# Kernel tuning notes

Hardware: AMD Instinct MI355X
Metric: run time of the kernel (lower is better)

## Reference

```python
import jax, jax.numpy as jnp
import numpy as np

B, P, C, F = 16, 1000, 91, 1024      # images, proposals/img, classes (incl bg), box-head dim
H, W = 800, 800                      # image shape (all images same size)
SCORE_THRESH = 0.05
NMS_THRESH = 0.5
DETS = 100                           # detections_per_img
MIN_SIZE = 1e-2
BBOX_XFORM_CLIP = float(np.log(1000.0 / 16.0))
OFF = float(max(H, W) + 2)           # class offset unit for batched (class-aware) NMS


def setup_inputs() -> dict:
    key = jax.random.key(0)
    k1, k2, k3, k4 = jax.random.split(key, 4)
    box_features = jax.random.normal(k1, (B * P, F), jnp.float32)
    Wc = jax.random.normal(k2, (F, C), jnp.float32) * 0.02
    bc = jnp.zeros((C,), jnp.float32)
    Wb = jax.random.normal(k3, (F, C * 4), jnp.float32) * 0.02
    bb = jnp.zeros((C * 4,), jnp.float32)
    u = jax.random.uniform(k4, (B, P, 4), jnp.float32)
    x1 = u[..., 0] * (W * 0.8)
    y1 = u[..., 1] * (H * 0.8)
    x2 = x1 + 16.0 + u[..., 2] * (W * 0.2)
    y2 = y1 + 16.0 + u[..., 3] * (H * 0.2)
    proposals = jnp.stack([x1, y1, x2, y2], axis=-1)
    return dict(box_features=box_features, Wc=Wc, bc=bc, Wb=Wb, bb=bb,
                proposals=proposals)


def _decode_and_clip(regs, props):
    # regs: [N, C, 4] deltas; props: [N, 4] xyxy. bbox_reg_weights = (1,1,1,1).
    w = props[:, 2] - props[:, 0]
    h = props[:, 3] - props[:, 1]
    cx = props[:, 0] + 0.5 * w
    cy = props[:, 1] + 0.5 * h
    dx, dy = regs[..., 0], regs[..., 1]
    dw = jnp.minimum(regs[..., 2], BBOX_XFORM_CLIP)
    dh = jnp.minimum(regs[..., 3], BBOX_XFORM_CLIP)
    pcx = dx * w[:, None] + cx[:, None]
    pcy = dy * h[:, None] + cy[:, None]
    pw = jnp.exp(dw) * w[:, None]
    ph = jnp.exp(dh) * h[:, None]
    x1 = jnp.clip(pcx - 0.5 * pw, 0.0, float(W))
    y1 = jnp.clip(pcy - 0.5 * ph, 0.0, float(H))
    x2 = jnp.clip(pcx + 0.5 * pw, 0.0, float(W))
    y2 = jnp.clip(pcy + 0.5 * ph, 0.0, float(H))
    return jnp.stack([x1, y1, x2, y2], axis=-1)  # [N, C, 4]


def _iou_one_vs_all(box, boxes):
    ix1 = jnp.maximum(box[0], boxes[:, 0])
    iy1 = jnp.maximum(box[1], boxes[:, 1])
    ix2 = jnp.minimum(box[2], boxes[:, 2])
    iy2 = jnp.minimum(box[3], boxes[:, 3])
    inter = jnp.clip(ix2 - ix1, 0.0) * jnp.clip(iy2 - iy1, 0.0)
    a1 = (box[2] - box[0]) * (box[3] - box[1])
    a2 = (boxes[:, 2] - boxes[:, 0]) * (boxes[:, 3] - boxes[:, 1])
    return inter / (a1 + a2 - inter + 1e-9)


def _greedy_nms(boxes, scores):
    # boxes: [M,4] (class-offset), scores: [M] (-inf = filtered out).
    # Returns selected indices [DETS] and scores [DETS] (0 where no valid pick).
    def body(i, st):
        sc, sel, ss = st
        j = jnp.argmax(sc)
        s = sc[j]
        iou = _iou_one_vs_all(boxes[j], boxes)
        sc = jnp.where(iou > NMS_THRESH, -jnp.inf, sc)  # suppresses j itself too
        valid = s > 0.0
        sel = sel.at[i].set(jnp.where(valid, j.astype(jnp.int32), 0))
        ss = ss.at[i].set(jnp.where(valid, s, 0.0))
        return sc, sel, ss
    init = (scores, jnp.zeros((DETS,), jnp.int32), jnp.zeros((DETS,), jnp.float32))
    _, sel, ss = jax.lax.fori_loop(0, DETS, body, init)
    return sel, ss


def reference(box_features, Wc, bc, Wb, bb, proposals):
    # Box predictor (FastRCNNPredictor-style linear heads).
    class_logits = box_features @ Wc + bc                  # [B*P, C]
    box_regression = (box_features @ Wb + bb).reshape(-1, C, 4)
    # Decode per-class boxes against proposals, clip to image.
    pred = _decode_and_clip(box_regression, proposals.reshape(-1, 4))  # [B*P, C, 4]
    scores = jax.nn.softmax(class_logits, axis=-1)         # [B*P, C]
    # Drop background class 0; flatten (proposal, class) per image.
    M = P * (C - 1)
    boxes_all = pred[:, 1:, :].reshape(B, M, 4)
    scores_all = scores[:, 1:].reshape(B, M)
    labels_all = jnp.tile(jnp.arange(1, C, dtype=jnp.int32), P)  # [M]
    # Score threshold + remove tiny boxes (mask instead of dynamic filter).
    bw = boxes_all[..., 2] - boxes_all[..., 0]
    bh = boxes_all[..., 3] - boxes_all[..., 1]
    keep = (scores_all > SCORE_THRESH) & (bw >= MIN_SIZE) & (bh >= MIN_SIZE)
    scores_m = jnp.where(keep, scores_all, -jnp.inf)
    # Class-aware batched NMS via per-class coordinate offsets.
    boxes_off = boxes_all + (labels_all.astype(jnp.float32) * OFF)[None, :, None]
    sel, det_scores = jax.vmap(_greedy_nms)(boxes_off, scores_m)   # [B,DETS]
    det_boxes = jnp.take_along_axis(boxes_all, sel[..., None], axis=1)  # [B,DETS,4]
    det_labels = labels_all[sel]                                        # [B,DETS]
    valid = det_scores > 0.0
    det_boxes = det_boxes * valid[..., None]
    det_labels = jnp.where(valid, det_labels, 0)
    return det_boxes, det_scores, det_labels
```

## Files before the change

### kernel.cpp

```cpp
#include <hip/hip_runtime.h>
#include <hip/hip_bf16.h>
#include <math.h>

typedef unsigned long long ull;

#define BB_ 16
#define PP_ 1000
#define CC_ 91
#define FF_ 1024
#define DETS_ 100
#define CAP_ 2048
#define CAND_MAX (BB_ * CAP_)
#define SURV_CAP 2048
#define CLS_CAP 256
#define BLK_CAND 720
#define IMG_W 800.0f
#define IMG_H 800.0f
#define OFF_ 802.0f
#define SCORE_TH 0.05f
#define PRE_TH 0.047f
#define NMS_TH 0.5f
#define MIN_SZ 0.01f
#define BBOX_CLIP_D 4.135166556742356

__global__ __launch_bounds__(256) void wb_transpose(
    const float* __restrict__ Wb, float* __restrict__ Wbt)
{
    const int idx = blockIdx.x * 256 + threadIdx.x;
    if (idx >= CC_ * 4 * FF_) return;
    const int c = idx >> 12;
    const int j = (idx >> 10) & 3;
    const int k = idx & 1023;
    if (c < 1) { Wbt[idx] = 0.f; return; }
    Wbt[idx] = Wb[(size_t)k * (CC_ * 4) + 4 * c + j];
}

__global__ __launch_bounds__(512) void prepass_rows(
    const float* __restrict__ A, const float* __restrict__ Wc,
    const float* __restrict__ bc,
    int* __restrict__ rowlist, int* __restrict__ nrowsp)
{
    __shared__ union __align__(16) SM {
        struct { float Af[2][16][34]; float Bs[2][16][98]; } t;
        float Ssc[32][97];
    } sm;
    __shared__ float comb[256][12];

    const int tid = threadIdx.x;
    const int kg = tid >> 8;
    const int l = tid & 255;
    const int row0 = blockIdx.x * 32;
    const int kbase = kg * 512;
    const int ty2 = (l >> 4) * 2;
    const int tx6 = (l & 15) * 6;

    const int am = l >> 2;
    const int ak = (l & 3) * 4;
    const int bk = l >> 4;
    const int bn = (l & 15) * 6;

    float acc[2][6];
#pragma unroll
    for (int i = 0; i < 2; ++i)
#pragma unroll
        for (int j = 0; j < 6; ++j) acc[i][j] = 0.f;

    float4 avP = make_float4(0.f, 0.f, 0.f, 0.f);
    if (l < 128)
        avP = *reinterpret_cast<const float4*>(
            A + (size_t)(row0 + am) * FF_ + kbase + ak);
    float bvP[6];
#pragma unroll
    for (int jj = 0; jj < 6; ++jj) {
        const int c = bn + jj;
        bvP[jj] = (c < CC_) ? Wc[(size_t)(kbase + bk) * CC_ + c] : 0.f;
    }

    for (int k0 = 0; k0 < 512; k0 += 16) {
        if (l < 128) {
            sm.t.Af[kg][ak + 0][am] = avP.x;
            sm.t.Af[kg][ak + 1][am] = avP.y;
            sm.t.Af[kg][ak + 2][am] = avP.z;
            sm.t.Af[kg][ak + 3][am] = avP.w;
        }
#pragma unroll
        for (int jj = 0; jj < 6; ++jj) sm.t.Bs[kg][bk][bn + jj] = bvP[jj];

        const int kn = k0 + 16;
        if (kn < 512) {
            if (l < 128)
                avP = *reinterpret_cast<const float4*>(
                    A + (size_t)(row0 + am) * FF_ + kbase + kn + ak);
#pragma unroll
            for (int jj = 0; jj < 6; ++jj) {
                const int c = bn + jj;
                bvP[jj] = (c < CC_) ? Wc[(size_t)(kbase + kn + bk) * CC_ + c] : 0.f;
            }
        }
        __syncthreads();

#pragma unroll
        for (int k = 0; k < 16; ++k) {
            const float2 af = *reinterpret_cast<const float2*>(&sm.t.Af[kg][k][ty2]);
            const float2 b01 = *reinterpret_cast<const float2*>(&sm.t.Bs[kg][k][tx6 + 0]);
            const float2 b23 = *reinterpret_cast<const float2*>(&sm.t.Bs[kg][k][tx6 + 2]);
            const float2 b45 = *reinterpret_cast<const float2*>(&sm.t.Bs[kg][k][tx6 + 4]);
            const float a0 = af.x, a1 = af.y;
            acc[0][0] += a0 * b01.x; acc[0][1] += a0 * b01.y;
            acc[0][2] += a0 * b23.x; acc[0][3] += a0 * b23.y;
            acc[0][4] += a0 * b45.x; acc[0][5] += a0 * b45.y;
            acc[1][0] += a1 * b01.x; acc[1][1] += a1 * b01.y;
            acc[1][2] += a1 * b23.x; acc[1][3] += a1 * b23.y;
            acc[1][4] += a1 * b45.x; acc[1][5] += a1 * b45.y;
        }
        __syncthreads();
    }

    if (kg == 1) {
#pragma unroll
        for (int i = 0; i < 2; ++i)
#pragma unroll
            for (int j = 0; j < 6; ++j) comb[l][i * 6 + j] = acc[i][j];
    }
    __syncthreads();
    if (kg == 0) {
#pragma unroll
        for (int i = 0; i < 2; ++i)
#pragma unroll
            for (int j = 0; j < 6; ++j) {
                const int c = tx6 + j;
                if (c < CC_)
                    sm.Ssc[ty2 + i][c] = acc[i][j] + comb[l][i * 6 + j] + bc[c];
            }
    }
    __syncthreads();

    if (tid < 32) {
        float m_all = sm.Ssc[tid][0];
        float m_fg = -INFINITY;
        for (int c = 1; c < CC_; ++c) {
            const float lv = sm.Ssc[tid][c];
            m_all = fmaxf(m_all, lv);
            m_fg = fmaxf(m_fg, lv);
        }
        float denom = 0.f;
        for (int c = 0; c < CC_; ++c) denom += expf(sm.Ssc[tid][c] - m_all);
        const float maxsc = expf(m_fg - m_all) / denom;
        if (maxsc > PRE_TH) {
            const int pos = atomicAdd(nrowsp, 1);
            rowlist[pos] = row0 + tid;
        }
    }
}

template<bool USE_T>
__global__ __launch_bounds__(512) void logits_fp64_rows(
    const float* __restrict__ A, const float* __restrict__ Wc,
    const float* __restrict__ bc,
    const float* __restrict__ Wb, const float* __restrict__ Wbt,
    const float* __restrict__ bb, const float* __restrict__ props,
    const int* __restrict__ rowlist, const int* __restrict__ nrowsp,
    float* __restrict__ cs, int* __restrict__ clab,
    int* __restrict__ corig, int* __restrict__ cpidx,
    int* __restrict__ cnt,
    float* __restrict__ cx1, float* __restrict__ cy1,
    float* __restrict__ cx2, float* __restrict__ cy2)
{
    const int nr = *nrowsp;
    const int row0 = blockIdx.x * 8;
    if (row0 >= nr) return;

    __shared__ union __align__(16) SM {
        struct { float Af[2][16][12]; float Bs[2][16][98]; } t;
        struct { int cp[BLK_CAND]; int cc[BLK_CAND]; int cg[BLK_CAND]; } d;
    } sm;
    __shared__ __align__(16) double dcomb[256][3];
    __shared__ float Ssc[8][97];
    __shared__ int ncand;

    const int tid = threadIdx.x;
    const int kg = tid >> 8;
    const int l = tid & 255;
    const int kbase = kg * 512;
    const int r = l >> 5;
    const int c0 = (l & 31) * 3;

    if (tid == 0) ncand = 0;

    const int aslot = l >> 2;
    const int akq = (l & 3) * 4;
    const float* Arow = nullptr;
    if (l < 32) {
        const int ridx = min(row0 + aslot, nr - 1);
        Arow = A + (size_t)rowlist[ridx] * FF_ + kbase;
    }
    const int bk = l >> 4;
    const int bn = (l & 15) * 6;

    double acc[3] = {0.0, 0.0, 0.0};

    float4 avP = make_float4(0.f, 0.f, 0.f, 0.f);
    if (l < 32) avP = *reinterpret_cast<const float4*>(Arow + akq);
    float bvP[6];
#pragma unroll
    for (int jj = 0; jj < 6; ++jj) {
        const int c = bn + jj;
        bvP[jj] = (c < CC_) ? Wc[(size_t)(kbase + bk) * CC_ + c] : 0.f;
    }

    for (int k0 = 0; k0 < 512; k0 += 16) {
        if (l < 32) {
            sm.t.Af[kg][akq + 0][aslot] = avP.x;
            sm.t.Af[kg][akq + 1][aslot] = avP.y;
            sm.t.Af[kg][akq + 2][aslot] = avP.z;
            sm.t.Af[kg][akq + 3][aslot] = avP.w;
        }
#pragma unroll
        for (int jj = 0; jj < 6; ++jj) sm.t.Bs[kg][bk][bn + jj] = bvP[jj];

        const int kn = k0 + 16;
        if (kn < 512) {
            if (l < 32)
                avP = *reinterpret_cast<const float4*>(Arow + kn + akq);
#pragma unroll
            for (int jj = 0; jj < 6; ++jj) {
                const int c = bn + jj;
                bvP[jj] = (c < CC_) ? Wc[(size_t)(kbase + kn + bk) * CC_ + c] : 0.f;
            }
        }
        __syncthreads();

#pragma unroll
        for (int k = 0; k < 16; ++k) {
            const double a0 = (double)sm.t.Af[kg][k][r];
            const double b0 = (double)sm.t.Bs[kg][k][c0 + 0];
            const double b1 = (double)sm.t.Bs[kg][k][c0 + 1];
            const double b2 = (double)sm.t.Bs[kg][k][c0 + 2];
            acc[0] += a0 * b0;
            acc[1] += a0 * b1;
            acc[2] += a0 * b2;
        }
        __syncthreads();
    }

    if (kg == 1) {
#pragma unroll
        for (int j = 0; j < 3; ++j) dcomb[l][j] = acc[j];
    }
    __syncthreads();
    if (kg == 0) {
#pragma unroll
        for (int j = 0; j < 3; ++j) {
            const int c = c0 + j;
            if (c < CC_) {
                const double v = acc[j] + dcomb[l][j];
                Ssc[r][c] = __fadd_rn((float)v, bc[c]);
            }
        }
    }
    __syncthreads();

    {
        const int w = tid >> 6;
        const int lane = tid & 63;
        if (w < 8 && row0 + w < nr) {
            const int p = rowlist[row0 + w];
            const int b = p / PP_;
            const int pi = p - b * PP_;

            const float l1 = Ssc[w][lane];
            const float l2 = (lane < CC_ - 64) ? Ssc[w][lane + 64] : -INFINITY;
            float m = fmaxf(l1, l2);
#pragma unroll
            for (int off = 32; off > 0; off >>= 1)
                m = fmaxf(m, __shfl_xor(m, off));

            double d = exp((double)l1 - (double)m);
            if (lane < CC_ - 64) d += exp((double)l2 - (double)m);
#pragma unroll
            for (int off = 1; off < 64; off <<= 1)
                d += __shfl_xor(d, off);

#pragma unroll
            for (int q = 0; q < 2; ++q) {
                const int c = lane + q * 64;
                if (c >= 1 && c < CC_) {
                    const double sd = exp((double)Ssc[w][c] - (double)m) / d;
                    const float score = (float)sd;
                    if (score > SCORE_TH) {
                        const int pos = atomicAdd(&cnt[b], 1);
                        if (pos < CAP_) {
                            const int g = b * CAP_ + pos;
                            cs[g] = score;
                            clab[g] = c;
                            corig[g] = pi * (CC_ - 1) + (c - 1);
                            cpidx[g] = p;
                            const int slot = atomicAdd(&ncand, 1);
                            if (slot < BLK_CAND) {
                                sm.d.cp[slot] = p;
                                sm.d.cc[slot] = c;
                                sm.d.cg[slot] = g;
                            }
                        }
                    }
                }
            }
        }
    }
    __syncthreads();

    {
        const int w = tid >> 6;
        const int lane = tid & 63;
        const int nc = min(ncand, BLK_CAND);
        for (int ci = w; ci < nc; ci += 8) {
            const int p = sm.d.cp[ci];
            const int c = sm.d.cc[ci];
            const int g = sm.d.cg[ci];

            const float* fr = A + (size_t)p * FF_;
            double a0 = 0.0, a1 = 0.0, a2 = 0.0, a3 = 0.0;
            if (USE_T) {
                const float* w0 = Wbt + (size_t)c * 4096;
                for (int k = lane; k < FF_; k += 64) {
                    const double f = (double)fr[k];
                    a0 += f * (double)w0[k];
                    a1 += f * (double)w0[1024 + k];
                    a2 += f * (double)w0[2048 + k];
                    a3 += f * (double)w0[3072 + k];
                }
            } else {
                const float* wb0 = Wb + 4 * c;
                for (int k = lane; k < FF_; k += 64) {
                    const double f = (double)fr[k];
                    const float4 wv = *reinterpret_cast<const float4*>(
                        wb0 + (size_t)k * (CC_ * 4));
                    a0 += f * (double)wv.x; a1 += f * (double)wv.y;
                    a2 += f * (double)wv.z; a3 += f * (double)wv.w;
                }
            }
#pragma unroll
            for (int off = 32; off > 0; off >>= 1) {
                a0 += __shfl_xor(a0, off);
                a1 += __shfl_xor(a1, off);
                a2 += __shfl_xor(a2, off);
                a3 += __shfl_xor(a3, off);
            }

            if (lane == 0) {
                const float dx = __fadd_rn((float)a0, bb[4 * c + 0]);
                const float dy = __fadd_rn((float)a1, bb[4 * c + 1]);
                const float clipf = (float)BBOX_CLIP_D;
                const float dw = fminf(__fadd_rn((float)a2, bb[4 * c + 2]), clipf);
                const float dh = fminf(__fadd_rn((float)a3, bb[4 * c + 3]), clipf);

                const float px1 = props[(size_t)p * 4 + 0];
                const float py1 = props[(size_t)p * 4 + 1];
                const float px2 = props[(size_t)p * 4 + 2];
                const float py2 = props[(size_t)p * 4 + 3];
                const float wq = __fsub_rn(px2, px1);
                const float hq = __fsub_rn(py2, py1);
                const float cxq = __fadd_rn(px1, __fmul_rn(0.5f, wq));
                const float cyq = __fadd_rn(py1, __fmul_rn(0.5f, hq));

                const float pcx = __fadd_rn(__fmul_rn(dx, wq), cxq);
                const float pcy = __fadd_rn(__fmul_rn(dy, hq), cyq);
                const float ew = (float)exp((double)dw);
                const float eh = (float)exp((double)dh);
                const float pw = __fmul_rn(ew, wq);
                const float ph = __fmul_rn(eh, hq);

                const float hw = __fmul_rn(0.5f, pw);
                const float hh = __fmul_rn(0.5f, ph);
                const float bx1 = fminf(fmaxf(__fsub_rn(pcx, hw), 0.f), IMG_W);
                const float by1 = fminf(fmaxf(__fsub_rn(pcy, hh), 0.f), IMG_H);
                const float bx2 = fminf(fmaxf(__fadd_rn(pcx, hw), 0.f), IMG_W);
                const float by2 = fminf(fmaxf(__fadd_rn(pcy, hh), 0.f), IMG_H);

                cx1[g] = bx1; cy1[g] = by1; cx2[g] = bx2; cy2[g] = by2;
                if (!(__fsub_rn(bx2, bx1) >= MIN_SZ && __fsub_rn(by2, by1) >= MIN_SZ)) {
                    cs[g] = -INFINITY;
                }
            }
        }
    }
}

__global__ __launch_bounds__(64) void nms_class(
    const float* __restrict__ c_x1, const float* __restrict__ c_y1,
    const float* __restrict__ c_x2, const float* __restrict__ c_y2,
    const float* __restrict__ c_s, const int* __restrict__ c_lab,
    const int* __restrict__ c_orig, const int* __restrict__ cnt,
    ull* __restrict__ skey, float* __restrict__ sx1v, float* __restrict__ sy1v,
    float* __restrict__ sx2v, float* __restrict__ sy2v,
    int* __restrict__ slabv, int* __restrict__ scnt)
{
    const int blk = blockIdx.x;
    const int b = blk / (CC_ - 1);
    const int c = 1 + (blk - b * (CC_ - 1));
    const int lane = threadIdx.x;

    __shared__ ull kk[CLS_CAP];
    __shared__ float x1s[CLS_CAP], y1s[CLS_CAP], x2s[CLS_CAP], y2s[CLS_CAP];

    const int n = min(cnt[b], CAP_);

    int mcnt = 0;
    for (int i0 = 0; i0 < n; i0 += 64) {
        const int i = i0 + lane;
        bool take = false;
        float s = 0.f; int so = 0; int g = 0;
        if (i < n) {
            g = b * CAP_ + i;
            if (c_lab[g] == c) {
                s = c_s[g];
                if (s > 0.f) { take = true; so = c_orig[g]; }
            }
        }
        const ull bal = __ballot(take);
        if (take) {
            const int pos = mcnt + __popcll(bal & ((1ull << lane) - 1ull));
            if (pos < CLS_CAP) {
                kk[pos] = ((ull)__float_as_uint(s) << 32) |
                          (unsigned int)(0x7FFFFFFF - so);
                x1s[pos] = c_x1[g]; y1s[pos] = c_y1[g];
                x2s[pos] = c_x2[g]; y2s[pos] = c_y2[g];
            }
        }
        mcnt += (int)__popcll(bal);
    }
    mcnt = min(mcnt, CLS_CAP);
    if (mcnt == 0) return;
    __syncthreads();

    while (true) {
        ull best = 0ull;
        for (int i = lane; i < mcnt; i += 64) best = (kk[i] > best) ? kk[i] : best;
#pragma unroll
        for (int off = 32; off > 0; off >>= 1) {
            const ull o = __shfl_xor(best, off);
            best = (o > best) ? o : best;
        }
        if (best == 0ull) break;

        int wsl = -1;
        for (int i = lane; i < mcnt; i += 64) if (kk[i] == best) wsl = i;
        const ull bal = __ballot(wsl >= 0);
        const int wlane = (int)__ffsll((long long)bal) - 1;
        wsl = __shfl(wsl, wlane);

        const float wx1 = x1s[wsl], wy1 = y1s[wsl];
        const float wx2 = x2s[wsl], wy2 = y2s[wsl];

        if (lane == 0) {
            const int sp = atomicAdd(&scnt[b], 1);
            if (sp < SURV_CAP) {
                const int sg = b * SURV_CAP + sp;
                skey[sg] = best;
                sx1v[sg] = wx1; sy1v[sg] = wy1;
                sx2v[sg] = wx2; sy2v[sg] = wy2;
                slabv[sg] = c;
            }
        }

        const float off = __fmul_rn((float)c, OFF_);
        const float ax1 = __fadd_rn(wx1, off), ay1 = __fadd_rn(wy1, off);
        const float ax2 = __fadd_rn(wx2, off), ay2 = __fadd_rn(wy2, off);
        const float a1 = __fmul_rn(__fsub_rn(ax2, ax1), __fsub_rn(ay2, ay1));
        for (int i = lane; i < mcnt; i += 64) {
            if (kk[i] == 0ull) continue;
            const float bx1 = __fadd_rn(x1s[i], off), by1 = __fadd_rn(y1s[i], off);
            const float bx2 = __fadd_rn(x2s[i], off), by2 = __fadd_rn(y2s[i], off);
            const float ix1 = fmaxf(ax1, bx1), iy1 = fmaxf(ay1, by1);
            const float ix2 = fminf(ax2, bx2), iy2 = fminf(ay2, by2);
            const float inter = __fmul_rn(fmaxf(__fsub_rn(ix2, ix1), 0.f),
                                          fmaxf(__fsub_rn(iy2, iy1), 0.f));
            const float a2 = __fmul_rn(__fsub_rn(bx2, bx1), __fsub_rn(by2, by1));
            const float den = __fadd_rn(__fsub_rn(__fadd_rn(a1, a2), inter), 1e-9f);
            const float iou = __fdiv_rn(inter, den);
            if (iou > NMS_TH) kk[i] = 0ull;
        }
        __syncthreads();
    }
}

__global__ __launch_bounds__(256) void nms_merge(
    const ull* __restrict__ skey, const float* __restrict__ sx1v,
    const float* __restrict__ sy1v, const float* __restrict__ sx2v,
    const float* __restrict__ sy2v, const int* __restrict__ slabv,
    const int* __restrict__ scnt, float* __restrict__ out)
{
    const int b = blockIdx.x;
    const int t = threadIdx.x;

    __shared__ ull k_[SURV_CAP];
    __shared__ int id_[SURV_CAP];

    const int m = min(scnt[b], SURV_CAP);
    int N2 = 128;
    while (N2 < m) N2 <<= 1;

    for (int i = t; i < N2; i += 256) {
        k_[i] = (i < m) ? skey[b * SURV_CAP + i] : 0ull;
        id_[i] = i;
    }
    __syncthreads();

    for (int ksz = 2; ksz <= N2; ksz <<= 1) {
        for (int j = ksz >> 1; j > 0; j >>= 1) {
            for (int i = t; i < N2; i += 256) {
                const int ixj = i ^ j;
                if (ixj > i) {
                    const ull a = k_[i], cc = k_[ixj];
                    const bool desc = ((i & ksz) == 0);
                    if (desc ? (a < cc) : (a > cc)) {
                        k_[i] = cc; k_[ixj] = a;
                        const int tmp = id_[i]; id_[i] = id_[ixj]; id_[ixj] = tmp;
                    }
                }
            }
            __syncthreads();
        }
    }

    const int boxes_base = 0;
    const int scores_base = BB_ * DETS_ * 4;
    const int labels_base = BB_ * DETS_ * 5;

    for (int r = t; r < DETS_; r += 256) {
        const ull key = (r < N2) ? k_[r] : 0ull;
        float* bo = out + boxes_base + (size_t)(b * DETS_ + r) * 4;
        if (key != 0ull) {
            const int sg = b * SURV_CAP + id_[r];
            bo[0] = sx1v[sg]; bo[1] = sy1v[sg];
            bo[2] = sx2v[sg]; bo[3] = sy2v[sg];
            out[scores_base + b * DETS_ + r] = __uint_as_float((unsigned)(key >> 32));
            out[labels_base + b * DETS_ + r] = (float)slabv[sg];
        } else {
            bo[0] = 0.f; bo[1] = 0.f; bo[2] = 0.f; bo[3] = 0.f;
            out[scores_base + b * DETS_ + r] = 0.f;
            out[labels_base + b * DETS_ + r] = 0.f;
        }
    }
}

extern "C" void kernel_launch(void* const* d_in, const int* in_sizes, int n_in,
                              void* d_out, int out_size, void* d_ws, size_t ws_size,
                              hipStream_t stream)
{
    const float* feat  = (const float*)d_in[0];
    const float* Wc    = (const float*)d_in[1];
    const float* bc    = (const float*)d_in[2];
    const float* Wb    = (const float*)d_in[3];
    const float* bb    = (const float*)d_in[4];
    const float* props = (const float*)d_in[5];
    for (int i = 0; i < n_in; ++i) {
        const float* q = (const float*)d_in[i];
        switch (in_sizes[i]) {
            case 16384000: feat  = q; break;
            case 93184:    Wc    = q; break;
            case 91:       bc    = q; break;
            case 372736:   Wb    = q; break;
            case 364:      bb    = q; break;
            case 64000:    props = q; break;
        }
    }
    float* out = (float*)d_out;

    char* ws = (char*)d_ws;
    int*   cnt    = (int*)ws;
    int*   scnt   = (int*)(ws + 64);
    int*   nrowsp = (int*)(ws + 128);
    float* cs    = (float*)(ws + 256);
    int*   clab  = (int*)(cs + CAND_MAX);
    int*   corig = clab + CAND_MAX;
    int*   cpidx = corig + CAND_MAX;
    float* cx1   = (float*)(cpidx + CAND_MAX);
    float* cy1   = cx1 + CAND_MAX;
    float* cx2   = cy1 + CAND_MAX;
    float* cy2   = cx2 + CAND_MAX;
    ull*   skey  = (ull*)(cy2 + CAND_MAX);
    float* sx1v  = (float*)(skey + (size_t)BB_ * SURV_CAP);
    float* sy1v  = sx1v + (size_t)BB_ * SURV_CAP;
    float* sx2v  = sy1v + (size_t)BB_ * SURV_CAP;
    float* sy2v  = sx2v + (size_t)BB_ * SURV_CAP;
    int*   slabv = (int*)(sy2v + (size_t)BB_ * SURV_CAP);
    int*   rowlist = slabv + (size_t)BB_ * SURV_CAP;
    float* Wbt   = (float*)(rowlist + 16384);

    const size_t need = ((char*)(Wbt + CC_ * 4 * FF_)) - ws;
    const bool useT = (ws_size >= need);

    hipMemsetAsync(ws, 0, 256, stream);

    if (useT)
        wb_transpose<<<(CC_ * 4 * FF_ + 255) / 256, 256, 0, stream>>>(Wb, Wbt);

    prepass_rows<<<BB_ * PP_ / 32, 512, 0, stream>>>(feat, Wc, bc,
        rowlist, nrowsp);

    if (useT)
        logits_fp64_rows<true><<<BB_ * PP_ / 8, 512, 0, stream>>>(
            feat, Wc, bc, Wb, Wbt, bb, props, rowlist, nrowsp,
            cs, clab, corig, cpidx, cnt, cx1, cy1, cx2, cy2);
    else
        logits_fp64_rows<false><<<BB_ * PP_ / 8, 512, 0, stream>>>(
            feat, Wc, bc, Wb, Wbt, bb, props, rowlist, nrowsp,
            cs, clab, corig, cpidx, cnt, cx1, cy1, cx2, cy2);

    nms_class<<<BB_ * (CC_ - 1), 64, 0, stream>>>(
        cx1, cy1, cx2, cy2, cs, clab, corig, cnt,
        skey, sx1v, sy1v, sx2v, sy2v, slabv, scnt);

    nms_merge<<<BB_, 256, 0, stream>>>(
        skey, sx1v, sy1v, sx2v, sy2v, slabv, scnt, out);
}
```

Baseline: 288.4 us.

## Use bf16 MFMA for prepass row filter with pre-transposed bf16 Wc

Replaces the fp32 SIMT tiled GEMM in the row prepass with bf16 MFMA 16x16x32 instructions. A new kernel first converts and transposes Wc to bf16, and activations are rounded to bf16 on load into shared memory. The pre-filter threshold is lowered so that the extra bf16 error does not drop rows that the exact fp64 logits pass would keep. The cost is an extra conversion kernel and more candidate rows reaching the expensive exact stage.

```diff
diff --git a/kernel.cpp b/kernel.cpp
--- a/kernel.cpp
+++ b/kernel.cpp
@@ -3,6 +3,8 @@
 #include <math.h>
 
 typedef unsigned long long ull;
+typedef __attribute__((ext_vector_type(8))) short bf16x8;
+typedef __attribute__((ext_vector_type(4))) float f32x4;
 
 #define BB_ 16
 #define PP_ 1000
@@ -18,7 +20,7 @@
 #define IMG_H 800.0f
 #define OFF_ 802.0f
 #define SCORE_TH 0.05f
-#define PRE_TH 0.047f
+#define PRE_TH 0.042f
 #define NMS_TH 0.5f
 #define MIN_SZ 0.01f
 #define BBOX_CLIP_D 4.135166556742356
@@ -35,103 +37,98 @@
     Wbt[idx] = Wb[(size_t)k * (CC_ * 4) + 4 * c + j];
 }
 
-__global__ __launch_bounds__(512) void prepass_rows(
-    const float* __restrict__ A, const float* __restrict__ Wc,
+__global__ __launch_bounds__(256) void wc_bf16_t(
+    const float* __restrict__ Wc, ushort* __restrict__ Wct)
+{
+    const int idx = blockIdx.x * 256 + threadIdx.x;
+    if (idx >= 96 * FF_) return;
+    const int c = idx >> 10, k = idx & 1023;
+    const float v = (c < CC_) ? Wc[(size_t)k * CC_ + c] : 0.f;
+    const unsigned u = __float_as_uint(v);
+    Wct[idx] = (ushort)((u + 0x8000u) >> 16);
+}
+
+__global__ __launch_bounds__(256) void prepass_mfma(
+    const float* __restrict__ A, const ushort* __restrict__ Wct,
     const float* __restrict__ bc,
     int* __restrict__ rowlist, int* __restrict__ nrowsp)
 {
     __shared__ union __align__(16) SM {
-        struct { float Af[2][16][34]; float Bs[2][16][98]; } t;
+        struct { ushort As[32][40]; ushort Bt[96][40]; } t;
         float Ssc[32][97];
     } sm;
-    __shared__ float comb[256][12];
 
     const int tid = threadIdx.x;
-    const int kg = tid >> 8;
-    const int l = tid & 255;
     const int row0 = blockIdx.x * 32;
-    const int kbase = kg * 512;
-    const int ty2 = (l >> 4) * 2;
-    const int tx6 = (l & 15) * 6;
-
-    const int am = l >> 2;
-    const int ak = (l & 3) * 4;
-    const int bk = l >> 4;
-    const int bn = (l & 15) * 6;
-
-    float acc[2][6];
-#pragma unroll
-    for (int i = 0; i < 2; ++i)
-#pragma unroll
-        for (int j = 0; j < 6; ++j) acc[i][j] = 0.f;
-
-    float4 avP = make_float4(0.f, 0.f, 0.f, 0.f);
-    if (l < 128)
-        avP = *reinterpret_cast<const float4*>(
-            A + (size_t)(row0 + am) * FF_ + kbase + ak);
-    float bvP[6];
-#pragma unroll
-    for (int jj = 0; jj < 6; ++jj) {
-        const int c = bn + jj;
-        bvP[jj] = (c < CC_) ? Wc[(size_t)(kbase + bk) * CC_ + c] : 0.f;
-    }
-
-    for (int k0 = 0; k0 < 512; k0 += 16) {
-        if (l < 128) {
-            sm.t.Af[kg][ak + 0][am] = avP.x;
-            sm.t.Af[kg][ak + 1][am] = avP.y;
-            sm.t.Af[kg][ak + 2][am] = avP.z;
-            sm.t.Af[kg][ak + 3][am] = avP.w;
-        }
-#pragma unroll
-        for (int jj = 0; jj < 6; ++jj) sm.t.Bs[kg][bk][bn + jj] = bvP[jj];
-
-        const int kn = k0 + 16;
-        if (kn < 512) {
-            if (l < 128)
-                avP = *reinterpret_cast<const float4*>(
-                    A + (size_t)(row0 + am) * FF_ + kbase + kn + ak);
-#pragma unroll
-            for (int jj = 0; jj < 6; ++jj) {
-                const int c = bn + jj;
-                bvP[jj] = (c < CC_) ? Wc[(size_t)(kbase + kn + bk) * CC_ + c] : 0.f;
+    const int lane = tid & 63;
+    const int w = tid >> 6;
+    const int rowOff = (w & 1) * 16;
+    const int colOff = (w >> 1) * 48;
+
+    const int arow = tid >> 3;
+    const int ak4 = (tid & 7) * 4;
+    const int bcol = tid >> 1;
+    const int bkh = (tid & 1) * 16;
+
+    f32x4 acc0 = {0.f, 0.f, 0.f, 0.f};
+    f32x4 acc1 = {0.f, 0.f, 0.f, 0.f};
+    f32x4 acc2 = {0.f, 0.f, 0.f, 0.f};
+
+    float4 avP = *(const float4*)(A + (size_t)(row0 + arow) * FF_ + ak4);
+    uint4 bvP0 = make_uint4(0, 0, 0, 0), bvP1 = make_uint4(0, 0, 0, 0);
+    if (tid < 192) {
+        const ushort* src = Wct + (size_t)bcol * FF_ + bkh;
+        bvP0 = *(const uint4*)(src);
+        bvP1 = *(const uint4*)(src + 8);
+    }
+
+    for (int k0 = 0; k0 < FF_; k0 += 32) {
+        {
+            const unsigned b0 = __float_as_uint(avP.x), b1 = __float_as_uint(avP.y);
+            const unsigned b2 = __float_as_uint(avP.z), b3 = __float_as_uint(avP.w);
+            const unsigned u0 = ((b0 + 0x8000u) >> 16) | (((b1 + 0x8000u) >> 16) << 16);
+            const unsigned u1 = ((b2 + 0x8000u) >> 16) | (((b3 + 0x8000u) >> 16) << 16);
+            *(uint2*)&sm.t.As[arow][ak4] = make_uint2(u0, u1);
+        }
+        if (tid < 192) {
+            *(uint4*)&sm.t.Bt[bcol][bkh] = bvP0;
+            *(uint4*)&sm.t.Bt[bcol][bkh + 8] = bvP1;
+        }
+
+        const int kn = k0 + 32;
+        if (kn < FF_) {
+            avP = *(const float4*)(A + (size_t)(row0 + arow) * FF_ + kn + ak4);
+            if (tid < 192) {
+                const ushort* src = Wct + (size_t)bcol * FF_ + kn + bkh;
+                bvP0 = *(const uint4*)(src);
+                bvP1 = *(const uint4*)(src + 8);
             }
         }
         __syncthreads();
 
-#pragma unroll
-        for (int k = 0; k < 16; ++k) {
-            const float2 af = *reinterpret_cast<const float2*>(&sm.t.Af[kg][k][ty2]);
-            const float2 b01 = *reinterpret_cast<const float2*>(&sm.t.Bs[kg][k][tx6 + 0]);
-            const float2 b23 = *reinterpret_cast<const float2*>(&sm.t.Bs[kg][k][tx6 + 2]);
-            const float2 b45 = *reinterpret_cast<const float2*>(&sm.t.Bs[kg][k][tx6 + 4]);
-            const float a0 = af.x, a1 = af.y;
-            acc[0][0] += a0 * b01.x; acc[0][1] += a0 * b01.y;
-            acc[0][2] += a0 * b23.x; acc[0][3] += a0 * b23.y;
-            acc[0][4] += a0 * b45.x; acc[0][5] += a0 * b45.y;
-            acc[1][0] += a1 * b01.x; acc[1][1] += a1 * b01.y;
-            acc[1][2] += a1 * b23.x; acc[1][3] += a1 * b23.y;
-            acc[1][4] += a1 * b45.x; acc[1][5] += a1 * b45.y;
-        }
+        const bf16x8 aF  = *(const bf16x8*)&sm.t.As[rowOff + (lane & 15)][(lane >> 4) * 8];
+        const bf16x8 bF0 = *(const bf16x8*)&sm.t.Bt[colOff +  0 + (lane & 15)][(lane >> 4) * 8];
+        const bf16x8 bF1 = *(const bf16x8*)&sm.t.Bt[colOff + 16 + (lane & 15)][(lane >> 4) * 8];
+        const bf16x8 bF2 = *(const bf16x8*)&sm.t.Bt[colOff + 32 + (lane & 15)][(lane >> 4) * 8];
+        acc0 = __builtin_amdgcn_mfma_f32_16x16x32_bf16(aF, bF0, acc0, 0, 0, 0);
+        acc1 = __builtin_amdgcn_mfma_f32_16x16x32_bf16(aF, bF1, acc1, 0, 0, 0);
+        acc2 = __builtin_amdgcn_mfma_f32_16x16x32_bf16(aF, bF2, acc2, 0, 0, 0);
         __syncthreads();
     }
 
-    if (kg == 1) {
-#pragma unroll
-        for (int i = 0; i < 2; ++i)
-#pragma unroll
-            for (int j = 0; j < 6; ++j) comb[l][i * 6 + j] = acc[i][j];
-    }
-    __syncthreads();
-    if (kg == 0) {
-#pragma unroll
-        for (int i = 0; i < 2; ++i)
-#pragma unroll
-            for (int j = 0; j < 6; ++j) {
-                const int c = tx6 + j;
-                if (c < CC_)
-                    sm.Ssc[ty2 + i][c] = acc[i][j] + comb[l][i * 6 + j] + bc[c];
-            }
+    {
+        const int r0 = rowOff + (lane >> 4) * 4;
+        const int cb = colOff + (lane & 15);
+#pragma unroll
+        for (int reg = 0; reg < 4; ++reg) {
+            const int row = r0 + reg;
+            int c = cb;
+            if (c < CC_) sm.Ssc[row][c] = acc0[reg] + bc[c];
+            c = cb + 16;
+            if (c < CC_) sm.Ssc[row][c] = acc1[reg] + bc[c];
+            c = cb + 32;
+            if (c < CC_) sm.Ssc[row][c] = acc2[reg] + bc[c];
+        }
     }
     __syncthreads();
 
@@ -586,17 +583,19 @@
     float* sy2v  = sx2v + (size_t)BB_ * SURV_CAP;
     int*   slabv = (int*)(sy2v + (size_t)BB_ * SURV_CAP);
     int*   rowlist = slabv + (size_t)BB_ * SURV_CAP;
-    float* Wbt   = (float*)(rowlist + 16384);
+    ushort* Wct  = (ushort*)(rowlist + 16384);
+    float* Wbt   = (float*)(Wct + 96 * FF_);
 
     const size_t need = ((char*)(Wbt + CC_ * 4 * FF_)) - ws;
     const bool useT = (ws_size >= need);
 
     hipMemsetAsync(ws, 0, 256, stream);
 
+    wc_bf16_t<<<(96 * FF_ + 255) / 256, 256, 0, stream>>>(Wc, Wct);
     if (useT)
         wb_transpose<<<(CC_ * 4 * FF_ + 255) / 256, 256, 0, stream>>>(Wb, Wbt);
 
-    prepass_rows<<<BB_ * PP_ / 32, 512, 0, stream>>>(feat, Wc, bc,
+    prepass_mfma<<<BB_ * PP_ / 32, 256, 0, stream>>>(feat, Wct, bc,
         rowlist, nrowsp);
 
     if (useT)
```

Result: faster. 251.0 us (-13.0%).
